# Kernel tuning notes

Measured on AMD Instinct MI355X. Metric: run time of the kernel, lower is better.

The kernel has to match this reference:

```python
import jax, jax.numpy as jnp
import numpy as np

NUM_USERS = 100000
NUM_ITEMS = 50000
NUM_EDGES = 4000000
EMB_DIM = 64
K_HOPS = 3


def setup_inputs() -> dict:
    key = jax.random.key(0)
    k1, k2, k3, k4, k5, k6 = jax.random.split(key, 6)
    N = NUM_USERS + NUM_ITEMS
    return {
        "users_emb": jax.random.normal(k1, (NUM_USERS, EMB_DIM), dtype=jnp.float32) * 0.1,
        "items_emb": jax.random.normal(k2, (NUM_ITEMS, EMB_DIM), dtype=jnp.float32) * 0.1,
        "edge_row": jax.random.randint(k3, (NUM_EDGES,), 0, N, dtype=jnp.int32),
        "edge_col": jax.random.randint(k4, (NUM_EDGES,), 0, N, dtype=jnp.int32),
        "user_id": jax.random.randint(k5, (4096,), 0, NUM_USERS, dtype=jnp.int32),
        "item_ids": jax.random.randint(k6, (4096,), 0, NUM_ITEMS, dtype=jnp.int32),
    }


def reference(users_emb, items_emb, edge_row, edge_col, user_id, item_ids):
    num_users = users_emb.shape[0]
    N = num_users + items_emb.shape[0]
    dt = users_emb.dtype

    # gcn_norm (no self loops): deg = rowsum of A, w_e = d_r^{-1/2} d_c^{-1/2}
    deg = jax.ops.segment_sum(jnp.ones(edge_row.shape[0], dtype=dt), edge_row,
                              num_segments=N)
    deg_inv_sqrt = jnp.where(deg > 0, 1.0 / jnp.sqrt(jnp.where(deg > 0, deg, 1.0)), 0.0)
    w = deg_inv_sqrt[edge_row] * deg_inv_sqrt[edge_col]  # [E]

    emb = jnp.concatenate([users_emb, items_emb], axis=0)  # [N, D]
    acc = emb  # running sum of K+1 layer snapshots
    for _ in range(K_HOPS):
        # SpMM: out[r] += w_e * emb[c]
        emb = jax.ops.segment_sum(w[:, None] * emb[edge_col], edge_row,
                                  num_segments=N)
        acc = acc + emb
    emb_final = acc / (K_HOPS + 1)  # layer-mean pooling

    users_final = emb_final[user_id]               # [B, D]
    items_final = emb_final[num_users + item_ids]  # [B, D]
    return jnp.concatenate([users_final, items_final], axis=1)  # [B, 2D]
```

## Files before the change

kernel.cpp:

```cpp
#include <hip/hip_runtime.h>
#include <hip/hip_bf16.h>

#define NUSERS 100000
#define NITEMS 50000
#define NN (NUSERS + NITEMS)
#define NE 4000000
#define DIM 64
#define BQ 4096
#define NBIN ((NN + 255) >> 8)
#define BINCAP 9216
#define EPB2 8192

typedef unsigned short u16;
typedef unsigned int u32;
typedef float v2f __attribute__((ext_vector_type(2)));
typedef unsigned u32x2 __attribute__((ext_vector_type(2)));

__device__ __forceinline__ float bf2f(u16 u) {
    return __uint_as_float(((unsigned)u) << 16);
}
__device__ __forceinline__ u16 f2bf(float f) {
    unsigned x = __float_as_uint(f);
    return (u16)((x + 0x7FFFu + ((x >> 16) & 1u)) >> 16);
}
__device__ __forceinline__ void add8p(v2f* acc2, uint4 u) {
    acc2[0] += (v2f){__uint_as_float(u.x << 16), __uint_as_float(u.x & 0xffff0000u)};
    acc2[1] += (v2f){__uint_as_float(u.y << 16), __uint_as_float(u.y & 0xffff0000u)};
    acc2[2] += (v2f){__uint_as_float(u.z << 16), __uint_as_float(u.z & 0xffff0000u)};
    acc2[3] += (v2f){__uint_as_float(u.w << 16), __uint_as_float(u.w & 0xffff0000u)};
}

#if __has_builtin(__builtin_amdgcn_update_dpp)
__device__ __forceinline__ float xadd8(float x) {
    int y = __builtin_amdgcn_update_dpp(0, __float_as_int(x), 0x128, 0xF, 0xF, true);
    return x + __int_as_float(y);
}
#else
__device__ __forceinline__ float xadd8(float x) { return x + __shfl_xor(x, 8, 64); }
#endif
#if __has_builtin(__builtin_amdgcn_permlane16_swap)
__device__ __forceinline__ float xadd16(float x) {
    u32x2 r = __builtin_amdgcn_permlane16_swap(__float_as_uint(x), __float_as_uint(x),
                                               false, false);
    return __uint_as_float(r.x) + __uint_as_float(r.y);
}
#else
__device__ __forceinline__ float xadd16(float x) { return x + __shfl_xor(x, 16, 64); }
#endif

#if __has_builtin(__builtin_amdgcn_sched_barrier)
#define SCHED_FENCE() __builtin_amdgcn_sched_barrier(0)
#else
#define SCHED_FENCE()
#endif

__device__ __forceinline__ void reduce_half(v2f* acc2) {
#pragma unroll
    for (int j = 0; j < 4; ++j) { acc2[j].x = xadd8(acc2[j].x);  acc2[j].y = xadd8(acc2[j].y);  }
#pragma unroll
    for (int j = 0; j < 4; ++j) { acc2[j].x = xadd16(acc2[j].x); acc2[j].y = xadd16(acc2[j].y); }
}

__device__ __forceinline__ void batch8(const int* __restrict__ col_s, int start,
                                       int s0, int lim, int eslot,
                                       const char* __restrict__ base2, v2f* acc2) {
    int cg[8];
#pragma unroll
    for (int g = 0; g < 8; ++g) {
        int slot = s0 + (g << 2) + eslot;
        int c = col_s[start + slot];
        cg[g] = (slot < lim) ? c : NN;
    }
    uint4 v[8];
#pragma unroll
    for (int g = 0; g < 8; ++g)
        v[g] = *(const uint4*)(base2 + (((u32)cg[g]) << 7));
    SCHED_FENCE();
#pragma unroll
    for (int g = 0; g < 8; ++g) add8p(acc2, v[g]);
}

template<bool MASKED>
__global__ void __launch_bounds__(256) k_spmm2(
        const int2* __restrict__ meta2, const int* __restrict__ col_s,
        const u16* __restrict__ in, u16* __restrict__ out,
        const unsigned char* __restrict__ mask) {
    int wid = (blockIdx.x * blockDim.x + threadIdx.x) >> 6;
    int lane = threadIdx.x & 63;
    int half = lane >> 5;
    int eslot = (lane >> 3) & 3;
    int dg = lane & 7;
    int r = (wid << 1) + half;
    int2 mv = meta2[r];
    int start = mv.x, n = mv.y;
    int m = MASKED ? (int)mask[r] : 1;
    int n8 = (n + 7) & ~7;
    int lim = m ? n8 : 0;
    if (MASKED && !__any(lim > 0)) return;
    const char* base2 = (const char*)in + (dg << 4);

    v2f acc2[4] = {(v2f)0.f, (v2f)0.f, (v2f)0.f, (v2f)0.f};
    batch8(col_s, start, 0, lim, eslot, base2, acc2);
    if (__any(lim > 32))
        batch8(col_s, start, 32, lim, eslot, base2, acc2);
    if (__any(lim > 64)) {
        for (int i = 64 + eslot; i < lim; i += 4) {
            int c = col_s[start + i];
            uint4 u = *(const uint4*)(base2 + (((u32)c) << 7));
            add8p(acc2, u);
        }
    }
    reduce_half(acc2);
    if (eslot == 0 && m) {
        float sc = (n > 0) ? (1.0f / (float)n) : 0.0f;
        v2f vs = {sc, sc};
        u32 p[4];
#pragma unroll
        for (int j = 0; j < 4; ++j) {
            v2f t = acc2[j] * vs;
            __hip_bfloat162 h = __float22bfloat162_rn(make_float2(t.x, t.y));
            p[j] = *(u32*)&h;
        }
        ((uint4*)out)[(size_t)r * 8 + dg] = make_uint4(p[0], p[1], p[2], p[3]);
    }
}

__global__ void __launch_bounds__(256) k_spmm_out2(
        const int2* __restrict__ meta2, const int* __restrict__ col_s,
        const u16* __restrict__ in, const int* __restrict__ uid,
        const int* __restrict__ iid, float* __restrict__ out) {
    int wid = (blockIdx.x * blockDim.x + threadIdx.x) >> 6;
    int lane = threadIdx.x & 63;
    int half = lane >> 5;
    int eslot = (lane >> 3) & 3;
    int dg = lane & 7;
    int q = (wid << 1) + half;
    int b, r, off;
    if (q < BQ) { b = q; r = uid[q]; off = 0; }
    else { b = q - BQ; r = NUSERS + iid[q - BQ]; off = DIM; }
    int2 mv = meta2[r];
    int start = mv.x, n = mv.y;
    int n8 = (n + 7) & ~7;
    const char* base2 = (const char*)in + (dg << 4);

    v2f acc2[4] = {(v2f)0.f, (v2f)0.f, (v2f)0.f, (v2f)0.f};
    batch8(col_s, start, 0, n8, eslot, base2, acc2);
    if (__any(n8 > 32))
        batch8(col_s, start, 32, n8, eslot, base2, acc2);
    if (__any(n8 > 64)) {
        for (int i = 64 + eslot; i < n8; i += 4) {
            int c = col_s[start + i];
            uint4 u = *(const uint4*)(base2 + (((u32)c) << 7));
            add8p(acc2, u);
        }
    }
    reduce_half(acc2);
    if (eslot == 0) {
        float dr = (n > 0) ? (1.0f / sqrtf((float)n)) : 0.0f;
        float* o = out + (size_t)b * (2 * DIM) + off + dg * 8;
#pragma unroll
        for (int j = 0; j < 4; ++j) {
            o[2 * j]     = (o[2 * j]     + dr * acc2[j].x) * 0.25f;
            o[2 * j + 1] = (o[2 * j + 1] + dr * acc2[j].y) * 0.25f;
        }
    }
}

__global__ void k_init(int* __restrict__ bin_cur, u32* __restrict__ m2w,
                       u16* __restrict__ ea, u16* __restrict__ eb) {
    int t = blockIdx.x * blockDim.x + threadIdx.x;
    if (t < NBIN) bin_cur[t] = t * BINCAP;
    if (t < 37504) m2w[t] = 0;
    if (t < 32) {
        ((u32*)(ea + (size_t)NN * DIM))[t] = 0;
        ((u32*)(eb + (size_t)NN * DIM))[t] = 0;
    }
}

__global__ void __launch_bounds__(1024) k_binA2(
        const int* __restrict__ row, const int* __restrict__ col,
        int* __restrict__ bin_cur, u32* __restrict__ pairs, int E) {
    __shared__ u32 stage[EPB2];
    __shared__ int hist[NBIN];
    __shared__ int base_l[NBIN];
    __shared__ int cbase[NBIN];
    __shared__ int lcur[NBIN];
    __shared__ int s[1024];
    int t = threadIdx.x;
    int base = blockIdx.x * EPB2;
    int lim = min(E - base, EPB2);

    if (t < NBIN) hist[t] = 0;
    __syncthreads();

    for (int i = t; i < lim; i += 1024)
        atomicAdd(&hist[row[base + i] >> 8], 1);
    __syncthreads();

    int v = (t < NBIN) ? hist[t] : 0;
    s[t] = v;
    __syncthreads();
    for (int off = 1; off < 1024; off <<= 1) {
        int x = (t >= off) ? s[t - off] : 0;
        __syncthreads();
        s[t] += x;
        __syncthreads();
    }
    if (t < NBIN) {
        int excl = s[t] - v;
        base_l[t] = excl;
        lcur[t] = excl;
        cbase[t] = (v > 0) ? atomicAdd(&bin_cur[t], v) : 0;
    }
    __syncthreads();

    for (int i = t; i < lim; i += 1024) {
        int r = row[base + i];
        int c = col[base + i];
        int pos = atomicAdd(&lcur[r >> 8], 1);
        stage[pos] = ((u32)(r & 255) << 24) | (u32)c;
    }
    __syncthreads();

    int wv = t >> 6;
    int lane = t & 63;
    for (int b = wv; b < NBIN; b += 16) {
        int h = hist[b];
        int lb = base_l[b];
        size_t gb = (size_t)cbase[b];
        for (int i = lane; i < h; i += 64)
            pairs[gb + i] = stage[lb + i];
    }
}

__global__ void __launch_bounds__(1024) k_binB(
        const u32* __restrict__ pairs, const int* __restrict__ bin_cur,
        int* __restrict__ col_s, int* __restrict__ rs, int* __restrict__ deg,
        int2* __restrict__ meta2) {
    __shared__ int cnt[256];
    __shared__ int pscan[256];
    __shared__ int cur[256];
    int b = blockIdx.x;
    int t = threadIdx.x;
    int base = b * BINCAP;
    int end = bin_cur[b];
    if (t < 256) cnt[t] = 0;
    __syncthreads();
    for (int i = base + t; i < end; i += 1024)
        atomicAdd(&cnt[pairs[i] >> 24], 1);
    __syncthreads();
    int v = (t < 256) ? cnt[t] : 0;
    int pv = (v + 7) & ~7;
    if (t < 256) pscan[t] = pv;
    __syncthreads();
    for (int off = 1; off < 256; off <<= 1) {
        int x = (t >= off && t < 256) ? pscan[t - off] : 0;
        __syncthreads();
        if (t < 256) pscan[t] += x;
        __syncthreads();
    }
    if (t < 256) {
        int rowstart = base + pscan[t] - pv;
        int r = (b << 8) + t;
        if (r < NN) {
            rs[r] = rowstart;
            deg[r] = v;
            meta2[r] = make_int2(rowstart, v);
        }
        cur[t] = rowstart;
        for (int i = v; i < pv; ++i) col_s[rowstart + i] = NN;
    }
    __syncthreads();
    for (int i = base + t; i < end; i += 1024) {
        u32 p = pairs[i];
        int pos = atomicAdd(&cur[p >> 24], 1);
        col_s[pos] = (int)(p & 0x00FFFFFFu);
    }
}

__global__ void k_concat_t0(const float* __restrict__ u, const float* __restrict__ it,
                            const int* __restrict__ deg, u16* __restrict__ emb) {
    int i = blockIdx.x * blockDim.x + threadIdx.x;
    const int NU4 = NUSERS * DIM / 4;
    const int NT4 = NN * DIM / 4;
    if (i >= NT4) return;
    int row = i >> 4;
    int d = deg[row];
    float sc = (d > 0) ? (1.0f / sqrtf((float)d)) : 0.0f;
    float4 v = (i < NU4) ? ((const float4*)u)[i] : ((const float4*)it)[i - NU4];
    ushort4 o;
    o.x = f2bf(sc * v.x); o.y = f2bf(sc * v.y);
    o.z = f2bf(sc * v.z); o.w = f2bf(sc * v.w);
    ((ushort4*)emb)[i] = o;
}

__global__ void k_mark(const int* __restrict__ uid, const int* __restrict__ iid,
                       const int* __restrict__ rs, const int* __restrict__ deg,
                       const int* __restrict__ col_s, unsigned char* __restrict__ m2) {
    int q = (blockIdx.x * blockDim.x + threadIdx.x) >> 6;
    if (q >= 2 * BQ) return;
    int lane = threadIdx.x & 63;
    int r = (q < BQ) ? uid[q] : (NUSERS + iid[q - BQ]);
    if (lane == 0) m2[r] = 1;
    int s = rs[r], n = deg[r];
    for (int i = lane; i < n; i += 64) m2[col_s[s + i]] = 1;
}


__global__ void k_gather_init(const int* __restrict__ uid, const int* __restrict__ iid,
                              const float* __restrict__ u, const float* __restrict__ it,
                              float* __restrict__ out) {
    int t = blockIdx.x * blockDim.x + threadIdx.x;
    if (t >= BQ * DIM) return;
    int b = t >> 6;
    int d = t & 63;
    out[b * (2 * DIM) + d]       = u[(size_t)uid[b] * DIM + d];
    out[b * (2 * DIM) + DIM + d] = it[(size_t)iid[b] * DIM + d];
}

__global__ void k_gather_add(const int* __restrict__ uid, const int* __restrict__ iid,
                             const int* __restrict__ deg, const u16* __restrict__ emb,
                             float* __restrict__ out) {
    int t = blockIdx.x * blockDim.x + threadIdx.x;
    if (t >= BQ * DIM) return;
    int b = t >> 6;
    int d = t & 63;
    int ru = uid[b];
    int ri = NUSERS + iid[b];
    int du = deg[ru], di = deg[ri];
    float su = (du > 0) ? sqrtf((float)du) : 0.0f;
    float si = (di > 0) ? sqrtf((float)di) : 0.0f;
    int ou = b * (2 * DIM) + d;
    int oi = ou + DIM;
    out[ou] = out[ou] + su * bf2f(emb[(size_t)ru * DIM + d]);
    out[oi] = out[oi] + si * bf2f(emb[(size_t)ri * DIM + d]);
}


extern "C" void kernel_launch(void* const* d_in, const int* in_sizes, int n_in,
                              void* d_out, int out_size, void* d_ws, size_t ws_size,
                              hipStream_t stream) {
    const float* users_emb = (const float*)d_in[0];
    const float* items_emb = (const float*)d_in[1];
    const int*   edge_row  = (const int*)d_in[2];
    const int*   edge_col  = (const int*)d_in[3];
    const int*   user_id   = (const int*)d_in[4];
    const int*   item_ids  = (const int*)d_in[5];
    float* out = (float*)d_out;

    char* ws = (char*)d_ws;
    int*   deg_i   = (int*)  (ws + 0);
    int*   rs      = (int*)  (ws + 655360);
    int*   bin_cur = (int*)  (ws + 1310720);
    unsigned char* m2 = (unsigned char*)(ws + 1400000);
    int2*  meta2   = (int2*) (ws + 2097152);
    int*   col_s   = (int*)  (ws + 4194304);
    u32*   pairs   = (u32*)  (ws + 29360128);
    u16*   emb_a   = (u16*)  (ws + 54525952);
    u16*   emb_b   = (u16*)  (ws + 75497472);

    k_init<<<147, 256, 0, stream>>>(bin_cur, (u32*)m2, emb_a, emb_b);

    k_binA2<<<(NE + EPB2 - 1) / EPB2, 1024, 0, stream>>>(edge_row, edge_col, bin_cur,
                                                         pairs, NE);
    k_binB<<<NBIN, 1024, 0, stream>>>(pairs, bin_cur, col_s, rs, deg_i, meta2);

    k_concat_t0<<<(NN * DIM / 4 + 255) / 256, 256, 0, stream>>>(users_emb, items_emb,
                                                                deg_i, emb_a);

    k_gather_init<<<(BQ * DIM + 255) / 256, 256, 0, stream>>>(user_id, item_ids,
                                                              users_emb, items_emb, out);

    k_mark<<<(2 * BQ + 3) / 4, 256, 0, stream>>>(user_id, item_ids, rs, deg_i, col_s, m2);

    k_spmm2<false><<<18750, 256, 0, stream>>>(meta2, col_s, emb_a, emb_b,
                                              (const unsigned char*)nullptr);
    k_gather_add<<<(BQ * DIM + 255) / 256, 256, 0, stream>>>(user_id, item_ids, deg_i,
                                                             emb_b, out);
    k_spmm2<true><<<18750, 256, 0, stream>>>(meta2, col_s, emb_b, emb_a, m2);
    k_gather_add<<<(BQ * DIM + 255) / 256, 256, 0, stream>>>(user_id, item_ids, deg_i,
                                                             emb_a, out);
    k_spmm_out2<<<1024, 256, 0, stream>>>(meta2, col_s, emb_a, user_id, item_ids, out);
}
```

Baseline: 296.3 us.

## Split bf16 embeddings into two 32-dim planes and run SpMM per plane

Stores the bf16 embedding table as two column planes of 32 dims (64 bytes per row) instead of one 128-byte row, and runs each SpMM pass twice, once per plane. Each plane is half the size of the full table, so the randomly gathered working set per pass is more likely to stay in L2 or the last-level cache. The lanes are remapped to 8 edge slots by 4 dim groups, with an extra DPP reduction step. The cost is twice as many kernel launches, reading col_s twice, and each gather being only 64 bytes wide.

```diff
diff --git a/kernel.cpp b/kernel.cpp
--- a/kernel.cpp
+++ b/kernel.cpp
@@ -10,6 +10,8 @@
 #define NBIN ((NN + 255) >> 8)
 #define BINCAP 9216
 #define EPB2 8192
+#define PLANE_U16 ((NN + 1) * 32)
+#define PLANE_BYTES ((NN + 1) * 64)
 
 typedef unsigned short u16;
 typedef unsigned int u32;
@@ -31,11 +33,16 @@
 }
 
 #if __has_builtin(__builtin_amdgcn_update_dpp)
+__device__ __forceinline__ float xadd4(float x) {
+    int y = __builtin_amdgcn_update_dpp(0, __float_as_int(x), 0x124, 0xF, 0xF, true);
+    return x + __int_as_float(y);
+}
 __device__ __forceinline__ float xadd8(float x) {
     int y = __builtin_amdgcn_update_dpp(0, __float_as_int(x), 0x128, 0xF, 0xF, true);
     return x + __int_as_float(y);
 }
 #else
+__device__ __forceinline__ float xadd4(float x) { return x + __shfl_xor(x, 4, 64); }
 __device__ __forceinline__ float xadd8(float x) { return x + __shfl_xor(x, 8, 64); }
 #endif
 #if __has_builtin(__builtin_amdgcn_permlane16_swap)
@@ -54,6 +61,15 @@
 #define SCHED_FENCE()
 #endif
 
+__device__ __forceinline__ void reduce_es(v2f* acc2) {
+#pragma unroll
+    for (int j = 0; j < 4; ++j) { acc2[j].x = xadd4(acc2[j].x);  acc2[j].y = xadd4(acc2[j].y);  }
+#pragma unroll
+    for (int j = 0; j < 4; ++j) { acc2[j].x = xadd8(acc2[j].x);  acc2[j].y = xadd8(acc2[j].y);  }
+#pragma unroll
+    for (int j = 0; j < 4; ++j) { acc2[j].x = xadd16(acc2[j].x); acc2[j].y = xadd16(acc2[j].y); }
+}
+
 __device__ __forceinline__ void reduce_half(v2f* acc2) {
 #pragma unroll
     for (int j = 0; j < 4; ++j) { acc2[j].x = xadd8(acc2[j].x);  acc2[j].y = xadd8(acc2[j].y);  }
@@ -61,9 +77,28 @@
     for (int j = 0; j < 4; ++j) { acc2[j].x = xadd16(acc2[j].x); acc2[j].y = xadd16(acc2[j].y); }
 }
 
-__device__ __forceinline__ void batch8(const int* __restrict__ col_s, int start,
+__device__ __forceinline__ void batchH(const int* __restrict__ col_s, int start,
                                        int s0, int lim, int eslot,
                                        const char* __restrict__ base2, v2f* acc2) {
+    int cg[4];
+#pragma unroll
+    for (int g = 0; g < 4; ++g) {
+        int slot = s0 + (g << 3) + eslot;
+        int c = col_s[start + slot];
+        cg[g] = (slot < lim) ? c : NN;
+    }
+    uint4 v[4];
+#pragma unroll
+    for (int g = 0; g < 4; ++g)
+        v[g] = *(const uint4*)(base2 + (((u32)cg[g]) << 6));
+    SCHED_FENCE();
+#pragma unroll
+    for (int g = 0; g < 4; ++g) add8p(acc2, v[g]);
+}
+
+__device__ __forceinline__ void batch8q(const int* __restrict__ col_s, int start,
+                                        int s0, int lim, int eslot,
+                                        const char* __restrict__ base2, v2f* acc2) {
     int cg[8];
 #pragma unroll
     for (int g = 0; g < 8; ++g) {
@@ -74,22 +109,22 @@
     uint4 v[8];
 #pragma unroll
     for (int g = 0; g < 8; ++g)
-        v[g] = *(const uint4*)(base2 + (((u32)cg[g]) << 7));
+        v[g] = *(const uint4*)(base2 + (((u32)cg[g]) << 6));
     SCHED_FENCE();
 #pragma unroll
     for (int g = 0; g < 8; ++g) add8p(acc2, v[g]);
 }
 
-template<bool MASKED>
-__global__ void __launch_bounds__(256) k_spmm2(
+template<int PASS, bool MASKED>
+__global__ void __launch_bounds__(256) k_spmmH(
         const int2* __restrict__ meta2, const int* __restrict__ col_s,
         const u16* __restrict__ in, u16* __restrict__ out,
         const unsigned char* __restrict__ mask) {
     int wid = (blockIdx.x * blockDim.x + threadIdx.x) >> 6;
     int lane = threadIdx.x & 63;
     int half = lane >> 5;
-    int eslot = (lane >> 3) & 3;
-    int dg = lane & 7;
+    int eslot = (lane >> 2) & 7;
+    int dg = lane & 3;
     int r = (wid << 1) + half;
     int2 mv = meta2[r];
     int start = mv.x, n = mv.y;
@@ -97,20 +132,20 @@
     int n8 = (n + 7) & ~7;
     int lim = m ? n8 : 0;
     if (MASKED && !__any(lim > 0)) return;
-    const char* base2 = (const char*)in + (dg << 4);
+    const char* base2 = (const char*)in + (u32)PASS * (u32)PLANE_BYTES + (dg << 4);
 
     v2f acc2[4] = {(v2f)0.f, (v2f)0.f, (v2f)0.f, (v2f)0.f};
-    batch8(col_s, start, 0, lim, eslot, base2, acc2);
+    batchH(col_s, start, 0, lim, eslot, base2, acc2);
     if (__any(lim > 32))
-        batch8(col_s, start, 32, lim, eslot, base2, acc2);
+        batchH(col_s, start, 32, lim, eslot, base2, acc2);
     if (__any(lim > 64)) {
-        for (int i = 64 + eslot; i < lim; i += 4) {
+        for (int i = 64 + eslot; i < lim; i += 8) {
             int c = col_s[start + i];
-            uint4 u = *(const uint4*)(base2 + (((u32)c) << 7));
+            uint4 u = *(const uint4*)(base2 + (((u32)c) << 6));
             add8p(acc2, u);
         }
     }
-    reduce_half(acc2);
+    reduce_es(acc2);
     if (eslot == 0 && m) {
         float sc = (n > 0) ? (1.0f / (float)n) : 0.0f;
         v2f vs = {sc, sc};
@@ -121,7 +156,8 @@
             __hip_bfloat162 h = __float22bfloat162_rn(make_float2(t.x, t.y));
             p[j] = *(u32*)&h;
         }
-        ((uint4*)out)[(size_t)r * 8 + dg] = make_uint4(p[0], p[1], p[2], p[3]);
+        ((uint4*)(out + (size_t)PASS * PLANE_U16))[(size_t)r * 4 + dg] =
+            make_uint4(p[0], p[1], p[2], p[3]);
     }
 }
 
@@ -141,16 +177,17 @@
     int2 mv = meta2[r];
     int start = mv.x, n = mv.y;
     int n8 = (n + 7) & ~7;
-    const char* base2 = (const char*)in + (dg << 4);
+    const char* base2 = (const char*)in + (u32)(dg >> 2) * (u32)PLANE_BYTES
+                      + ((dg & 3) << 4);
 
     v2f acc2[4] = {(v2f)0.f, (v2f)0.f, (v2f)0.f, (v2f)0.f};
-    batch8(col_s, start, 0, n8, eslot, base2, acc2);
+    batch8q(col_s, start, 0, n8, eslot, base2, acc2);
     if (__any(n8 > 32))
-        batch8(col_s, start, 32, n8, eslot, base2, acc2);
+        batch8q(col_s, start, 32, n8, eslot, base2, acc2);
     if (__any(n8 > 64)) {
         for (int i = 64 + eslot; i < n8; i += 4) {
             int c = col_s[start + i];
-            uint4 u = *(const uint4*)(base2 + (((u32)c) << 7));
+            uint4 u = *(const uint4*)(base2 + (((u32)c) << 6));
             add8p(acc2, u);
         }
     }
@@ -171,9 +208,11 @@
     int t = blockIdx.x * blockDim.x + threadIdx.x;
     if (t < NBIN) bin_cur[t] = t * BINCAP;
     if (t < 37504) m2w[t] = 0;
-    if (t < 32) {
-        ((u32*)(ea + (size_t)NN * DIM))[t] = 0;
-        ((u32*)(eb + (size_t)NN * DIM))[t] = 0;
+    if (t < 16) {
+        ((u32*)(ea + (size_t)NN * 32))[t] = 0;
+        ((u32*)(ea + (size_t)PLANE_U16 + (size_t)NN * 32))[t] = 0;
+        ((u32*)(eb + (size_t)NN * 32))[t] = 0;
+        ((u32*)(eb + (size_t)PLANE_U16 + (size_t)NN * 32))[t] = 0;
     }
 }
 
@@ -285,13 +324,16 @@
     const int NT4 = NN * DIM / 4;
     if (i >= NT4) return;
     int row = i >> 4;
+    int sub = i & 15;
     int d = deg[row];
     float sc = (d > 0) ? (1.0f / sqrtf((float)d)) : 0.0f;
     float4 v = (i < NU4) ? ((const float4*)u)[i] : ((const float4*)it)[i - NU4];
     ushort4 o;
     o.x = f2bf(sc * v.x); o.y = f2bf(sc * v.y);
     o.z = f2bf(sc * v.z); o.w = f2bf(sc * v.w);
-    ((ushort4*)emb)[i] = o;
+    int plane = sub >> 3;
+    int po = sub & 7;
+    ((ushort4*)(emb + (size_t)plane * PLANE_U16))[(size_t)row * 8 + po] = o;
 }
 
 __global__ void k_mark(const int* __restrict__ uid, const int* __restrict__ iid,
@@ -330,10 +372,12 @@
     int du = deg[ru], di = deg[ri];
     float su = (du > 0) ? sqrtf((float)du) : 0.0f;
     float si = (di > 0) ? sqrtf((float)di) : 0.0f;
+    size_t pb = (size_t)(d >> 5) * PLANE_U16;
+    int dd = d & 31;
     int ou = b * (2 * DIM) + d;
     int oi = ou + DIM;
-    out[ou] = out[ou] + su * bf2f(emb[(size_t)ru * DIM + d]);
-    out[oi] = out[oi] + si * bf2f(emb[(size_t)ri * DIM + d]);
+    out[ou] = out[ou] + su * bf2f(emb[pb + (size_t)ru * 32 + dd]);
+    out[oi] = out[oi] + si * bf2f(emb[pb + (size_t)ri * 32 + dd]);
 }
 
 
@@ -373,11 +417,14 @@
 
     k_mark<<<(2 * BQ + 3) / 4, 256, 0, stream>>>(user_id, item_ids, rs, deg_i, col_s, m2);
 
-    k_spmm2<false><<<18750, 256, 0, stream>>>(meta2, col_s, emb_a, emb_b,
-                                              (const unsigned char*)nullptr);
+    k_spmmH<0, false><<<18750, 256, 0, stream>>>(meta2, col_s, emb_a, emb_b,
+                                                 (const unsigned char*)nullptr);
+    k_spmmH<1, false><<<18750, 256, 0, stream>>>(meta2, col_s, emb_a, emb_b,
+                                                 (const unsigned char*)nullptr);
     k_gather_add<<<(BQ * DIM + 255) / 256, 256, 0, stream>>>(user_id, item_ids, deg_i,
                                                              emb_b, out);
-    k_spmm2<true><<<18750, 256, 0, stream>>>(meta2, col_s, emb_b, emb_a, m2);
+    k_spmmH<0, true><<<18750, 256, 0, stream>>>(meta2, col_s, emb_b, emb_a, m2);
+    k_spmmH<1, true><<<18750, 256, 0, stream>>>(meta2, col_s, emb_b, emb_a, m2);
     k_gather_add<<<(BQ * DIM + 255) / 256, 256, 0, stream>>>(user_id, item_ids, deg_i,
                                                              emb_a, out);
     k_spmm_out2<<<1024, 256, 0, stream>>>(meta2, col_s, emb_a, user_id, item_ids, out);
```

Measured after the change: 364.4 us. 23.0% more time.
